# Kernel optimization log

Measured on AMD Instinct MI355X. Metric: run time of the kernel, lower is better.

The kernel has to match this reference:

```python
import jax, jax.numpy as jnp
import numpy as np


def setup_inputs() -> dict:
    key = jax.random.key(0)
    ks = jax.random.split(key, 6)
    B, L, C = 32, 336, 512
    t = L // 2 + 1  # 169 rfft frequencies; four_l must equal t
    s = 1.0 / np.sqrt(C)
    return {
        "x": jax.random.normal(ks[0], (B, L, C), jnp.float32),
        "Wr": jax.random.normal(ks[1], (t, C, C), jnp.float32) * s,  # real part of complex Linear weights [t, out, in]
        "Wi": jax.random.normal(ks[2], (t, C, C), jnp.float32) * s,  # imag part
        "br": jax.random.normal(ks[3], (t, C), jnp.float32) * s,
        "bi": jax.random.normal(ks[4], (t, C), jnp.float32) * s,
        "weights": jax.random.normal(ks[5], (t,), jnp.float32),
    }


def reference(x, Wr, Wi, br, bi, weights):
    # x: [B, L, C] real. rfft along time with ortho norm -> [B, t, C] complex.
    B, L, C = x.shape
    t = Wr.shape[0]
    n = 2 * (t - 1)  # torch irfft default output length (== L, L even)
    xf = jnp.fft.rfft(x, axis=1, norm='ortho')  # [B, t, C] complex64

    # Per-frequency complex linear: y[b,i,o] = sum_c xf[b,i,c] * W[i,o,c] + b[i,o].
    # This fuses the original repeat + eye-mask + python loop into one batched GEMM.
    W = Wr + 1j * Wi
    b = br + 1j * bi
    y = jnp.einsum('bic,ioc->bio', xf, W) + b[None]  # [B, t, C]

    # The original builds fre[b,i,:,c] as a spectrum that is one-hot at frequency i
    # (value y[b,i,c]) and irffts along the frequency axis (ortho norm). For a one-hot
    # spectrum: irfft(onehot_i * y)[l] = scale_i * Re(y * exp(2*pi*j*i*l/n)) / sqrt(n),
    # with scale_i = 2 except at DC (i=0) and Nyquist (i=t-1) where it is 1
    # (imag parts of DC/Nyquist bins are discarded by C2R, matching torch).
    # Finally ConcatenationWithLearnableCoefficient sums over i with softmax weights,
    # so we fold softmax(weights) * scale_i / sqrt(n) into one coefficient per i.
    i_idx = jnp.arange(t)
    scale = jnp.where((i_idx == 0) | (i_idx == t - 1), 1.0, 2.0).astype(jnp.float32)
    w = jax.nn.softmax(weights)
    coef = w * scale / jnp.sqrt(jnp.float32(n))  # [t]

    l_idx = jnp.arange(n)
    theta = (2.0 * jnp.pi / n) * (i_idx[:, None] * l_idx[None, :]).astype(jnp.float32)  # [t, n]
    cos_m, sin_m = jnp.cos(theta), jnp.sin(theta)

    yr = y.real * coef[None, :, None]
    yi = y.imag * coef[None, :, None]
    # Re(y * e^{j theta}) = yr*cos - yi*sin ; sum over frequencies i -> [B, n, C]
    out = jnp.einsum('bic,il->blc', yr, cos_m) - jnp.einsum('bic,il->blc', yi, sin_m)
    return out
```

## Files before the change

### kernel.cpp

```cpp
#include <hip/hip_runtime.h>
#include <math.h>

typedef short   s16x8  __attribute__((ext_vector_type(8)));
typedef __bf16  bf16x8 __attribute__((ext_vector_type(8)));
typedef float   f32x4  __attribute__((ext_vector_type(4)));

#define T_FREQ 169
#define NN     336
#define CCH    512
#define BB     32
#define TP     176
#define LP     352
#define KP     192

static constexpr size_t OFF_COEF = 0;
static constexpr size_t OFF_FC   = 1024;
static constexpr size_t OFF_FS   = OFF_FC + 124928;
static constexpr size_t OFF_CCOS = OFF_FS + 124928;
static constexpr size_t OFF_CSIN = OFF_CCOS + 130048;
static constexpr size_t OFF_XT   = OFF_CSIN + 130048;
static constexpr size_t OFF_XR   = OFF_XT + (size_t)BB*CCH*LP*2;
static constexpr size_t OFF_XI   = OFF_XR + (size_t)TP*BB*CCH*2;
static constexpr size_t OFF_Y    = OFF_XI + (size_t)TP*BB*CCH*2;

__device__ __forceinline__ unsigned short f2bf(float f){
  return __builtin_bit_cast(unsigned short, (__bf16)f);
}

__device__ __forceinline__ bf16x8 cvt8(float4 lo, float4 hi){
  bf16x8 r;
  r[0]=(__bf16)lo.x; r[1]=(__bf16)lo.y; r[2]=(__bf16)lo.z; r[3]=(__bf16)lo.w;
  r[4]=(__bf16)hi.x; r[5]=(__bf16)hi.y; r[6]=(__bf16)hi.z; r[7]=(__bf16)hi.w;
  return r;
}

__device__ __forceinline__ f32x4 mfma16(bf16x8 a, bf16x8 b, f32x4 c){
  return __builtin_amdgcn_mfma_f32_16x16x32_bf16(a, b, c, 0, 0, 0);
}

__global__ __launch_bounds__(256) void prep_tables(const float* __restrict__ wts, char* ws){
  float* coef = (float*)(ws + OFF_COEF);
  unsigned short* Fc  = (unsigned short*)(ws + OFF_FC);
  unsigned short* Fs  = (unsigned short*)(ws + OFF_FS);
  unsigned short* Cc  = (unsigned short*)(ws + OFF_CCOS);
  unsigned short* Cs  = (unsigned short*)(ws + OFF_CSIN);
  const float PI2_N = 6.283185307179586f / (float)NN;
  const float inv_sqrt_n = 0.05455447255899809f;

  if (blockIdx.x == 0){
    __shared__ float red[256];
    int tid = threadIdx.x;
    float v = (tid < T_FREQ) ? wts[tid] : -1e30f;
    red[tid] = v; __syncthreads();
    for (int s = 128; s > 0; s >>= 1){ if (tid < s) red[tid] = fmaxf(red[tid], red[tid+s]); __syncthreads(); }
    float mx = red[0]; __syncthreads();
    float e = (tid < T_FREQ) ? expf(v - mx) : 0.f;
    red[tid] = e; __syncthreads();
    for (int s = 128; s > 0; s >>= 1){ if (tid < s) red[tid] += red[tid+s]; __syncthreads(); }
    float ssum = red[0];
    if (tid < T_FREQ){
      float sc = (tid == 0 || tid == T_FREQ-1) ? 1.f : 2.f;
      coef[tid] = (e / ssum) * sc * inv_sqrt_n;
    }
    return;
  }
  int gid = (blockIdx.x - 1) * 256 + threadIdx.x;
  int stride = (gridDim.x - 1) * 256;
  for (int e = gid; e < TP*LP; e += stride){
    int i = e / LP, l = e % LP;
    float c = 0.f, s = 0.f;
    if (l < NN){
      int m = (i * l) % NN;
      float sv, cv; sincosf(PI2_N * (float)m, &sv, &cv);
      c = cv * inv_sqrt_n; s = -sv * inv_sqrt_n;
    }
    Fc[e] = f2bf(c); Fs[e] = f2bf(s);
  }
  for (int e = gid; e < NN*KP; e += stride){
    int l = e / KP, i = e % KP;
    float c = 0.f, s = 0.f;
    if (i < T_FREQ){
      int m = (i * l) % NN;
      float sv, cv; sincosf(PI2_N * (float)m, &sv, &cv);
      c = cv; s = -sv;
    }
    Cc[e] = f2bf(c); Cs[e] = f2bf(s);
  }
}

__global__ __launch_bounds__(256) void transpose_x(const float* __restrict__ x, char* ws){
  unsigned short* xt = (unsigned short*)(ws + OFF_XT);
  __shared__ float tile[32][33];
  int bid = blockIdx.x;
  int b  = bid / (11*16);
  int rm = bid % (11*16);
  int lt = rm / 16, ct = rm % 16;
  int tx = threadIdx.x & 31, ty = threadIdx.x >> 5;
  #pragma unroll
  for (int k = 0; k < 4; ++k){
    int l = lt*32 + ty + k*8;
    int c = ct*32 + tx;
    float v = (l < NN) ? x[((size_t)b*NN + l)*CCH + c] : 0.f;
    tile[ty + k*8][tx] = v;
  }
  __syncthreads();
  #pragma unroll
  for (int k = 0; k < 4; ++k){
    int crow = ct*32 + ty + k*8;
    int lcol = lt*32 + tx;
    xt[((size_t)b*CCH + crow)*LP + lcol] = f2bf(tile[tx][ty + k*8]);
  }
}

__global__ __launch_bounds__(256) void stage_rfft(char* ws){
  const unsigned short* xt = (const unsigned short*)(ws + OFF_XT);
  const unsigned short* Fc = (const unsigned short*)(ws + OFF_FC);
  const unsigned short* Fs = (const unsigned short*)(ws + OFF_FS);
  unsigned short* xr = (unsigned short*)(ws + OFF_XR);
  unsigned short* xi = (unsigned short*)(ws + OFF_XI);

  int bid = blockIdx.x;
  int b  = bid >> 4;
  int rm = bid & 15;
  int c0 = (rm & 7) * 64;
  int mh = rm >> 3;
  int mbase = mh * 5;
  int tid = threadIdx.x, lane = tid & 63, wv = tid >> 6;
  int kg = lane >> 4, ln = lane & 15;
  int c = c0 + wv*16 + ln;

  f32x4 aR[6], aI[6];
  #pragma unroll
  for (int m = 0; m < 6; ++m){ aR[m] = (f32x4){0,0,0,0}; aI[m] = (f32x4){0,0,0,0}; }

  const unsigned short* xrow = xt + ((size_t)b*CCH + c)*LP;
  for (int kk = 0; kk < 11; ++kk){
    int ko = kk*32 + kg*8;
    bf16x8 bx = *(const bf16x8*)(xrow + ko);
    #pragma unroll
    for (int m = 0; m < 6; ++m){
      bf16x8 fc = *(const bf16x8*)(Fc + (size_t)((mbase+m)*16 + ln)*LP + ko);
      bf16x8 fs = *(const bf16x8*)(Fs + (size_t)((mbase+m)*16 + ln)*LP + ko);
      aR[m] = mfma16(fc, bx, aR[m]);
      aI[m] = mfma16(fs, bx, aI[m]);
    }
  }
  int rbase = kg*4;
  #pragma unroll
  for (int m = 0; m < 6; ++m){
    #pragma unroll
    for (int r = 0; r < 4; ++r){
      int i = (mbase+m)*16 + rbase + r;
      size_t off = ((size_t)i*BB + b)*CCH + c;
      xr[off] = f2bf(aR[m][r]);
      xi[off] = f2bf(aI[m][r]);
    }
  }
}

#define CGEMM_COMPUTE(W0,W1,V0,V1,KK) do {                                   \
    int ko_ = (KK)*32 + kb;                                                  \
    bf16x8 ar0 = *(const bf16x8*)(xrb + (size_t)(ln)*CCH + ko_);             \
    bf16x8 ar1 = *(const bf16x8*)(xrb + (size_t)(16+ln)*CCH + ko_);          \
    bf16x8 ai0 = *(const bf16x8*)(xib + (size_t)(ln)*CCH + ko_);             \
    bf16x8 ai1 = *(const bf16x8*)(xib + (size_t)(16+ln)*CCH + ko_);          \
    bf16x8 bwr = cvt8(W0,W1);                                                \
    bf16x8 bwi = cvt8(V0,V1);                                                \
    bf16x8 bwin = __builtin_bit_cast(bf16x8,                                 \
        (s16x8)(__builtin_bit_cast(s16x8,bwi) ^ (short)0x8000));             \
    accR0 = mfma16(ar0, bwr,  accR0);                                        \
    accR0 = mfma16(ai0, bwin, accR0);                                        \
    accI0 = mfma16(ar0, bwi,  accI0);                                        \
    accI0 = mfma16(ai0, bwr,  accI0);                                        \
    accR1 = mfma16(ar1, bwr,  accR1);                                        \
    accR1 = mfma16(ai1, bwin, accR1);                                        \
    accI1 = mfma16(ar1, bwi,  accI1);                                        \
    accI1 = mfma16(ai1, bwr,  accI1);                                        \
  } while (0)

__global__ __launch_bounds__(256) void stage_cgemm(const float* __restrict__ Wr, const float* __restrict__ Wi,
                                                   const float* __restrict__ br, const float* __restrict__ bi,
                                                   char* ws){
  const unsigned short* xr = (const unsigned short*)(ws + OFF_XR);
  const unsigned short* xi = (const unsigned short*)(ws + OFF_XI);
  const float* coef = (const float*)(ws + OFF_COEF);
  unsigned int* y = (unsigned int*)(ws + OFF_Y);

  int i  = blockIdx.x >> 3;
  int nb = blockIdx.x & 7;
  int tid = threadIdx.x, lane = tid & 63, wv = tid >> 6;
  int kg = lane >> 4, ln = lane & 15;
  int o = nb*64 + wv*16 + ln;
  int kb = kg*8;

  f32x4 accR0 = (f32x4){0,0,0,0}, accR1 = (f32x4){0,0,0,0};
  f32x4 accI0 = (f32x4){0,0,0,0}, accI1 = (f32x4){0,0,0,0};

  const float* wrk = Wr + (size_t)i*CCH*CCH + (size_t)o*CCH + kb;
  const float* wik = Wi + (size_t)i*CCH*CCH + (size_t)o*CCH + kb;
  const unsigned short* xrb = xr + (size_t)i*BB*CCH;
  const unsigned short* xib = xi + (size_t)i*BB*CCH;

  float4 pa0, pa1, pb0, pb1, qa0, qa1, qb0, qb1;
  pa0 = *(const float4*)(wrk);     pa1 = *(const float4*)(wrk + 4);
  pb0 = *(const float4*)(wik);     pb1 = *(const float4*)(wik + 4);

  #pragma unroll
  for (int kk = 0; kk < 16; kk += 2){
    {
      const float* wr1 = wrk + (size_t)(kk+1)*32;
      const float* wi1 = wik + (size_t)(kk+1)*32;
      qa0 = *(const float4*)(wr1); qa1 = *(const float4*)(wr1 + 4);
      qb0 = *(const float4*)(wi1); qb1 = *(const float4*)(wi1 + 4);
    }
    CGEMM_COMPUTE(pa0, pa1, pb0, pb1, kk);
    if (kk + 2 < 16){
      const float* wr2 = wrk + (size_t)(kk+2)*32;
      const float* wi2 = wik + (size_t)(kk+2)*32;
      pa0 = *(const float4*)(wr2); pa1 = *(const float4*)(wr2 + 4);
      pb0 = *(const float4*)(wi2); pb1 = *(const float4*)(wi2 + 4);
    }
    CGEMM_COMPUTE(qa0, qa1, qb0, qb1, kk+1);
  }

  float cf  = coef[i];
  float fbr = br[(size_t)i*CCH + o];
  float fbi = bi[(size_t)i*CCH + o];
  #pragma unroll
  for (int r = 0; r < 4; ++r){
    int bb0 = kg*4 + r;
    float vr0 = (accR0[r] + fbr) * cf;
    float vi0 = (accI0[r] + fbi) * cf;
    y[((size_t)bb0*KP + i)*CCH + o] = (unsigned)f2bf(vr0) | ((unsigned)f2bf(vi0) << 16);
    int bb1 = 16 + kg*4 + r;
    float vr1 = (accR1[r] + fbr) * cf;
    float vi1 = (accI1[r] + fbi) * cf;
    y[((size_t)bb1*KP + i)*CCH + o] = (unsigned)f2bf(vr1) | ((unsigned)f2bf(vi1) << 16);
  }
}

__global__ __launch_bounds__(256) void stage_irfft(const char* ws_c, float* __restrict__ out){
  const char* ws = ws_c;
  const unsigned short* Cc = (const unsigned short*)(ws + OFF_CCOS);
  const unsigned short* Cs = (const unsigned short*)(ws + OFF_CSIN);
  const unsigned int* y = (const unsigned int*)(ws + OFF_Y);

  __shared__ unsigned short lr[64][40];
  __shared__ unsigned short li[64][40];

  int bid = blockIdx.x;
  int b  = bid >> 4;
  int rm = bid & 15;
  int c0 = (rm & 7) * 64;
  int mh = rm >> 3;
  int mbase = mh * 10;
  int tid = threadIdx.x, lane = tid & 63, wv = tid >> 6;
  int kg = lane >> 4, ln = lane & 15;

  f32x4 acc[11];
  #pragma unroll
  for (int m = 0; m < 11; ++m) acc[m] = (f32x4){0,0,0,0};

  for (int kk = 0; kk < 6; ++kk){
    if (kk) __syncthreads();
    #pragma unroll
    for (int q = 0; q < 8; ++q){
      int idx = q*256 + tid;
      int ir = idx >> 6, cc = idx & 63;
      int i = kk*32 + ir;
      unsigned u = (i < T_FREQ) ? y[((size_t)b*KP + i)*CCH + c0 + cc] : 0u;
      lr[cc][ir] = (unsigned short)(u & 0xffffu);
      li[cc][ir] = (unsigned short)(u >> 16);
    }
    __syncthreads();
    int ko = kk*32 + kg*8;
    bf16x8 blr = *(const bf16x8*)(&lr[wv*16 + ln][kg*8]);
    bf16x8 bli = *(const bf16x8*)(&li[wv*16 + ln][kg*8]);
    #pragma unroll
    for (int m = 0; m < 11; ++m){
      bf16x8 ac = *(const bf16x8*)(Cc + (size_t)((mbase+m)*16 + ln)*KP + ko);
      bf16x8 as = *(const bf16x8*)(Cs + (size_t)((mbase+m)*16 + ln)*KP + ko);
      acc[m] = mfma16(ac, blr, acc[m]);
      acc[m] = mfma16(as, bli, acc[m]);
    }
  }

  int cdst = c0 + wv*16 + ln;
  #pragma unroll
  for (int m = 0; m < 11; ++m){
    #pragma unroll
    for (int r = 0; r < 4; ++r){
      int l = (mbase+m)*16 + kg*4 + r;
      out[((size_t)b*NN + l)*CCH + cdst] = acc[m][r];
    }
  }
}

extern "C" void kernel_launch(void* const* d_in, const int* in_sizes, int n_in,
                              void* d_out, int out_size, void* d_ws, size_t ws_size,
                              hipStream_t stream){
  const float* x   = (const float*)d_in[0];
  const float* Wr  = (const float*)d_in[1];
  const float* Wi  = (const float*)d_in[2];
  const float* br  = (const float*)d_in[3];
  const float* bi  = (const float*)d_in[4];
  const float* wts = (const float*)d_in[5];
  char* ws = (char*)d_ws;

  prep_tables<<<257, 256, 0, stream>>>(wts, ws);
  transpose_x<<<32*11*16, 256, 0, stream>>>(x, ws);
  stage_rfft<<<512, 256, 0, stream>>>(ws);
  stage_cgemm<<<T_FREQ*8, 256, 0, stream>>>(Wr, Wi, br, bi, ws);
  stage_irfft<<<512, 256, 0, stream>>>(ws, (float*)d_out);
}
```

Measured before the change: 190.8 us.

## Stage complex weights through swizzled LDS and split cgemm across more blocks

The complex GEMM kernel now runs 32 blocks per frequency instead of 8. Each block loads a 16-row slice of Wr and Wi with coalesced row-wise reads, converts it to bf16, and stores it in LDS with an XOR swizzle. The four waves then split the work by batch half and by real or imaginary output, so each wave keeps a single accumulator. The output y is split into separate real and imaginary bf16 planes, which changes how the irfft stage reads it: two 16-bit loads per element instead of one packed 32-bit load. The aim is more parallelism and better coalescing of the dominant weight stream, at the cost of an LDS round trip and a sync per block.

```diff
diff --git a/kernel.cpp b/kernel.cpp
--- a/kernel.cpp
+++ b/kernel.cpp
@@ -21,7 +21,8 @@
 static constexpr size_t OFF_XT   = OFF_CSIN + 130048;
 static constexpr size_t OFF_XR   = OFF_XT + (size_t)BB*CCH*LP*2;
 static constexpr size_t OFF_XI   = OFF_XR + (size_t)TP*BB*CCH*2;
-static constexpr size_t OFF_Y    = OFF_XI + (size_t)TP*BB*CCH*2;
+static constexpr size_t OFF_YR   = OFF_XI + (size_t)TP*BB*CCH*2;
+static constexpr size_t OFF_YI   = OFF_YR + (size_t)BB*KP*CCH*2;
 
 __device__ __forceinline__ unsigned short f2bf(float f){
   return __builtin_bit_cast(unsigned short, (__bf16)f);
@@ -158,84 +159,77 @@
   }
 }
 
-#define CGEMM_COMPUTE(W0,W1,V0,V1,KK) do {                                   \
-    int ko_ = (KK)*32 + kb;                                                  \
-    bf16x8 ar0 = *(const bf16x8*)(xrb + (size_t)(ln)*CCH + ko_);             \
-    bf16x8 ar1 = *(const bf16x8*)(xrb + (size_t)(16+ln)*CCH + ko_);          \
-    bf16x8 ai0 = *(const bf16x8*)(xib + (size_t)(ln)*CCH + ko_);             \
-    bf16x8 ai1 = *(const bf16x8*)(xib + (size_t)(16+ln)*CCH + ko_);          \
-    bf16x8 bwr = cvt8(W0,W1);                                                \
-    bf16x8 bwi = cvt8(V0,V1);                                                \
-    bf16x8 bwin = __builtin_bit_cast(bf16x8,                                 \
-        (s16x8)(__builtin_bit_cast(s16x8,bwi) ^ (short)0x8000));             \
-    accR0 = mfma16(ar0, bwr,  accR0);                                        \
-    accR0 = mfma16(ai0, bwin, accR0);                                        \
-    accI0 = mfma16(ar0, bwi,  accI0);                                        \
-    accI0 = mfma16(ai0, bwr,  accI0);                                        \
-    accR1 = mfma16(ar1, bwr,  accR1);                                        \
-    accR1 = mfma16(ai1, bwin, accR1);                                        \
-    accI1 = mfma16(ar1, bwi,  accI1);                                        \
-    accI1 = mfma16(ai1, bwr,  accI1);                                        \
-  } while (0)
-
-__global__ __launch_bounds__(256) void stage_cgemm(const float* __restrict__ Wr, const float* __restrict__ Wi,
-                                                   const float* __restrict__ br, const float* __restrict__ bi,
-                                                   char* ws){
+__global__ __launch_bounds__(256, 4) void stage_cgemm(const float* __restrict__ Wr, const float* __restrict__ Wi,
+                                                      const float* __restrict__ br, const float* __restrict__ bi,
+                                                      char* ws){
   const unsigned short* xr = (const unsigned short*)(ws + OFF_XR);
   const unsigned short* xi = (const unsigned short*)(ws + OFF_XI);
   const float* coef = (const float*)(ws + OFF_COEF);
-  unsigned int* y = (unsigned int*)(ws + OFF_Y);
-
-  int i  = blockIdx.x >> 3;
-  int nb = blockIdx.x & 7;
+  unsigned short* yr = (unsigned short*)(ws + OFF_YR);
+  unsigned short* yi = (unsigned short*)(ws + OFF_YI);
+
+  __shared__ unsigned short sW[2][16*CCH];
+
+  int bid = blockIdx.x;
+  int i  = bid >> 5;
+  int ot = bid & 31;
   int tid = threadIdx.x, lane = tid & 63, wv = tid >> 6;
   int kg = lane >> 4, ln = lane & 15;
-  int o = nb*64 + wv*16 + ln;
-  int kb = kg*8;
-
-  f32x4 accR0 = (f32x4){0,0,0,0}, accR1 = (f32x4){0,0,0,0};
-  f32x4 accI0 = (f32x4){0,0,0,0}, accI1 = (f32x4){0,0,0,0};
-
-  const float* wrk = Wr + (size_t)i*CCH*CCH + (size_t)o*CCH + kb;
-  const float* wik = Wi + (size_t)i*CCH*CCH + (size_t)o*CCH + kb;
-  const unsigned short* xrb = xr + (size_t)i*BB*CCH;
-  const unsigned short* xib = xi + (size_t)i*BB*CCH;
-
-  float4 pa0, pa1, pb0, pb1, qa0, qa1, qb0, qb1;
-  pa0 = *(const float4*)(wrk);     pa1 = *(const float4*)(wrk + 4);
-  pb0 = *(const float4*)(wik);     pb1 = *(const float4*)(wik + 4);
-
-  #pragma unroll
-  for (int kk = 0; kk < 16; kk += 2){
-    {
-      const float* wr1 = wrk + (size_t)(kk+1)*32;
-      const float* wi1 = wik + (size_t)(kk+1)*32;
-      qa0 = *(const float4*)(wr1); qa1 = *(const float4*)(wr1 + 4);
-      qb0 = *(const float4*)(wi1); qb1 = *(const float4*)(wi1 + 4);
-    }
-    CGEMM_COMPUTE(pa0, pa1, pb0, pb1, kk);
-    if (kk + 2 < 16){
-      const float* wr2 = wrk + (size_t)(kk+2)*32;
-      const float* wi2 = wik + (size_t)(kk+2)*32;
-      pa0 = *(const float4*)(wr2); pa1 = *(const float4*)(wr2 + 4);
-      pb0 = *(const float4*)(wi2); pb1 = *(const float4*)(wi2 + 4);
-    }
-    CGEMM_COMPUTE(qa0, qa1, qb0, qb1, kk+1);
-  }
-
-  float cf  = coef[i];
-  float fbr = br[(size_t)i*CCH + o];
-  float fbi = bi[(size_t)i*CCH + o];
+
+  const float* gWr = Wr + ((size_t)i*CCH + ot*16)*CCH;
+  const float* gWi = Wi + ((size_t)i*CCH + ot*16)*CCH;
+  float4 buf[16];
+  #pragma unroll
+  for (int j = 0; j < 4; ++j){
+    int row = j*4 + wv;
+    const float* s = gWr + (size_t)row*CCH + lane*8;
+    buf[2*j]   = *(const float4*)(s);
+    buf[2*j+1] = *(const float4*)(s + 4);
+  }
+  #pragma unroll
+  for (int j = 0; j < 4; ++j){
+    int row = j*4 + wv;
+    const float* s = gWi + (size_t)row*CCH + lane*8;
+    buf[8+2*j]   = *(const float4*)(s);
+    buf[8+2*j+1] = *(const float4*)(s + 4);
+  }
+  #pragma unroll
+  for (int j = 0; j < 4; ++j){
+    int row = j*4 + wv;
+    int dst = row*CCH + ((lane ^ (row & 7)) << 3);
+    *(bf16x8*)&sW[0][dst] = cvt8(buf[2*j],   buf[2*j+1]);
+    *(bf16x8*)&sW[1][dst] = cvt8(buf[8+2*j], buf[8+2*j+1]);
+  }
+  __syncthreads();
+
+  int mb = wv & 1, part = wv >> 1;
+  f32x4 acc = (f32x4){0,0,0,0};
+  const unsigned short* xa = xr + (size_t)(i*BB + mb*16 + ln)*CCH;
+  const unsigned short* xb = xi + (size_t)(i*BB + mb*16 + ln)*CCH;
+
+  #pragma unroll
+  for (int kk = 0; kk < 16; ++kk){
+    int ko = kk*32 + kg*8;
+    bf16x8 ar = *(const bf16x8*)(xa + ko);
+    bf16x8 ai = *(const bf16x8*)(xb + ko);
+    int g = (((kk*4 + kg) ^ (ln & 7)) << 3);
+    bf16x8 wr8 = *(const bf16x8*)&sW[0][ln*CCH + g];
+    bf16x8 wi8 = *(const bf16x8*)&sW[1][ln*CCH + g];
+    bf16x8 nwi = __builtin_bit_cast(bf16x8, (s16x8)(__builtin_bit_cast(s16x8, wi8) ^ (short)0x8000));
+    bf16x8 b1 = part ? wi8 : wr8;
+    bf16x8 b2 = part ? wr8 : nwi;
+    acc = mfma16(ar, b1, acc);
+    acc = mfma16(ai, b2, acc);
+  }
+
+  int o = ot*16 + ln;
+  float cf = coef[i];
+  float bias = (part ? bi : br)[(size_t)i*CCH + o];
+  unsigned short* yp = part ? yi : yr;
   #pragma unroll
   for (int r = 0; r < 4; ++r){
-    int bb0 = kg*4 + r;
-    float vr0 = (accR0[r] + fbr) * cf;
-    float vi0 = (accI0[r] + fbi) * cf;
-    y[((size_t)bb0*KP + i)*CCH + o] = (unsigned)f2bf(vr0) | ((unsigned)f2bf(vi0) << 16);
-    int bb1 = 16 + kg*4 + r;
-    float vr1 = (accR1[r] + fbr) * cf;
-    float vi1 = (accI1[r] + fbi) * cf;
-    y[((size_t)bb1*KP + i)*CCH + o] = (unsigned)f2bf(vr1) | ((unsigned)f2bf(vi1) << 16);
+    int bb = mb*16 + kg*4 + r;
+    yp[((size_t)bb*KP + i)*CCH + o] = f2bf((acc[r] + bias) * cf);
   }
 }
 
@@ -243,7 +237,8 @@
   const char* ws = ws_c;
   const unsigned short* Cc = (const unsigned short*)(ws + OFF_CCOS);
   const unsigned short* Cs = (const unsigned short*)(ws + OFF_CSIN);
-  const unsigned int* y = (const unsigned int*)(ws + OFF_Y);
+  const unsigned short* yr = (const unsigned short*)(ws + OFF_YR);
+  const unsigned short* yi = (const unsigned short*)(ws + OFF_YI);
 
   __shared__ unsigned short lr[64][40];
   __shared__ unsigned short li[64][40];
@@ -268,9 +263,13 @@
       int idx = q*256 + tid;
       int ir = idx >> 6, cc = idx & 63;
       int i = kk*32 + ir;
-      unsigned u = (i < T_FREQ) ? y[((size_t)b*KP + i)*CCH + c0 + cc] : 0u;
-      lr[cc][ir] = (unsigned short)(u & 0xffffu);
-      li[cc][ir] = (unsigned short)(u >> 16);
+      unsigned short vr = 0, vi = 0;
+      if (i < T_FREQ){
+        size_t off = ((size_t)b*KP + i)*CCH + c0 + cc;
+        vr = yr[off]; vi = yi[off];
+      }
+      lr[cc][ir] = vr;
+      li[cc][ir] = vi;
     }
     __syncthreads();
     int ko = kk*32 + kg*8;
@@ -310,6 +309,6 @@
   prep_tables<<<257, 256, 0, stream>>>(wts, ws);
   transpose_x<<<32*11*16, 256, 0, stream>>>(x, ws);
   stage_rfft<<<512, 256, 0, stream>>>(ws);
-  stage_cgemm<<<T_FREQ*8, 256, 0, stream>>>(Wr, Wi, br, bi, ws);
+  stage_cgemm<<<T_FREQ*32, 256, 0, stream>>>(Wr, Wi, br, bi, ws);
   stage_irfft<<<512, 256, 0, stream>>>(ws, (float*)d_out);
 }
```

Result: slower. 201.8 us (+5.8%).
